# Kernel tuning notes

Hardware: AMD Instinct MI355X
Metric: run time of the kernel (lower is better)

Reference implementation:

```python
import jax, jax.numpy as jnp
import numpy as np

NUM_HEADS = 4
CATEGORY_SIZE = 128
DIM = 192
B, N, M = 2, 65000, 64


def setup_inputs() -> dict:
    key = jax.random.key(0)
    k1, k2, k3, k4 = jax.random.split(key, 4)
    qkv = jax.random.normal(k1, (B, N, 3 * DIM), dtype=jnp.float32)
    sim = jax.random.normal(k2, (B, N, M), dtype=jnp.float32)
    proj_w = jax.random.normal(k3, (DIM, DIM), dtype=jnp.float32) * (1.0 / np.sqrt(DIM))
    proj_b = jax.random.normal(k4, (DIM,), dtype=jnp.float32) * 0.01
    logit_scale = jnp.log(10.0 * jnp.ones((1, 1), dtype=jnp.float32))
    return {"qkv": qkv, "sim": sim, "proj_w": proj_w, "proj_b": proj_b,
            "logit_scale": logit_scale, "x_size": 65000}


def reference(qkv, sim, proj_w, proj_b, logit_scale, x_size):
    b, n, c3 = qkv.shape
    c = c3 // 3
    h = NUM_HEADS
    gs = min(n, CATEGORY_SIZE)
    ng = (n + gs - 1) // gs
    pad_n = ng * gs - n

    # token -> category id, then sort tokens by category
    tk_id = jnp.argmax(sim, axis=-1)                      # (b, n) int
    sort_idx = jnp.argsort(tk_id, axis=-1)                # (b, n)
    inv_idx = jnp.argsort(sort_idx, axis=-1)              # inverse permutation

    shuffled = jnp.take_along_axis(qkv, sort_idx[..., None], axis=1)  # (b, n, 3c)
    if pad_n > 0:
        pad = jnp.flip(shuffled[:, n - pad_n:n, :], axis=1)
        shuffled = jnp.concatenate([shuffled, pad], axis=1)           # (b, n+pad_n, 3c)

    # (3, b, ng, h, gs, c/h)
    y = shuffled.reshape(b, ng, gs, 3, h, c // h).transpose(3, 0, 1, 4, 2, 5)
    q, k, v = y[0], y[1], y[2]

    scale = jnp.exp(jnp.minimum(logit_scale, jnp.log(jnp.asarray(100.0, dtype=qkv.dtype))))
    attn = jnp.einsum('bghqd,bghkd->bghqk', q, k) * scale  # (b, ng, h, gs, gs)
    attn = jax.nn.softmax(attn, axis=-1)
    out = jnp.einsum('bghqk,bghkd->bghqd', attn, v)        # (b, ng, h, gs, c/h)
    out = out.transpose(0, 1, 3, 2, 4).reshape(b, n + pad_n, c)[:, :n, :]

    # scatter back to original token order
    out = jnp.take_along_axis(out, inv_idx[..., None], axis=1)
    return out @ proj_w.T + proj_b
```

## Files before the change

### kernel.cpp

```cpp
#include <hip/hip_runtime.h>
#include <hip/hip_bf16.h>
#include <math.h>

#define BB 2
#define NN 65000
#define MM 64
#define DIM 192
#define NH 4
#define HD 48
#define GS 128
#define NG 508
#define SORT_TPB 256
#define NBLK 254

#define NROWS_PAD 130048
#define NROWTILES 2032

typedef __attribute__((ext_vector_type(8))) short bf16x8;
typedef __attribute__((ext_vector_type(8))) _Float16 f16x8;
typedef __attribute__((ext_vector_type(2))) __fp16 fp16x2;
typedef __attribute__((ext_vector_type(4))) float f32x4;
typedef __attribute__((ext_vector_type(16))) float f32x16;
typedef __attribute__((ext_vector_type(8))) unsigned short u16x8;

__device__ __forceinline__ unsigned short f2bf(float f) {
  __hip_bfloat16 h = __float2bfloat16(f);
  return *(unsigned short*)&h;
}
__device__ __forceinline__ unsigned int pkh(float lo, float hi) {
  fp16x2 t = __builtin_amdgcn_cvt_pkrtz(lo, hi);
  return *(unsigned int*)&t;
}
__device__ __forceinline__ f16x8 cvt8h(float4 a, float4 b) {
  f16x8 r;
  r[0] = (_Float16)a.x; r[1] = (_Float16)a.y; r[2] = (_Float16)a.z; r[3] = (_Float16)a.w;
  r[4] = (_Float16)b.x; r[5] = (_Float16)b.y; r[6] = (_Float16)b.z; r[7] = (_Float16)b.w;
  return r;
}
__device__ __forceinline__ void gload_lds16(const float* src, float* lds_dst) {
  __builtin_amdgcn_global_load_lds(
      (const __attribute__((address_space(1))) unsigned int*)src,
      (__attribute__((address_space(3))) unsigned int*)lds_dst, 16, 0, 0);
}

__global__ void k_argmax_hist(const float* __restrict__ sim, int* __restrict__ tk,
                              int* __restrict__ hist) {
  __shared__ int cnt[MM];
  const int b = blockIdx.y, blk = blockIdx.x;
  if (threadIdx.x < MM) cnt[threadIdx.x] = 0;
  __syncthreads();
  int t = blk * SORT_TPB + threadIdx.x;
  if (t < NN) {
    const float4* row = (const float4*)(sim + ((size_t)b * NN + t) * MM);
    float best = -INFINITY;
    int bi = 0;
#pragma unroll
    for (int j = 0; j < MM / 4; ++j) {
      float4 v = row[j];
      if (v.x > best) { best = v.x; bi = 4 * j + 0; }
      if (v.y > best) { best = v.y; bi = 4 * j + 1; }
      if (v.z > best) { best = v.z; bi = 4 * j + 2; }
      if (v.w > best) { best = v.w; bi = 4 * j + 3; }
    }
    tk[b * NN + t] = bi;
    atomicAdd(&cnt[bi], 1);
  }
  __syncthreads();
  if (threadIdx.x < MM)
    hist[(b * NBLK + blk) * MM + threadIdx.x] = cnt[threadIdx.x];
}

__global__ void k_scan(const int* __restrict__ hist, int* __restrict__ boff) {
  const int b = blockIdx.x;
  const int tid = threadIdx.x;
  const int seg = tid >> 6, bin = tid & 63;
  __shared__ int part[4][MM];
  __shared__ int basev[MM];
  const int lo = seg * 64, hi = (seg == 3) ? NBLK : (lo + 64);
  int s = 0;
  for (int blk = lo; blk < hi; ++blk) s += hist[(b * NBLK + blk) * MM + bin];
  part[seg][bin] = s;
  __syncthreads();
  if (tid < 64) {
    int tot = part[0][bin] + part[1][bin] + part[2][bin] + part[3][bin];
    int incl = tot;
#pragma unroll
    for (int d = 1; d < 64; d <<= 1) {
      int o = __shfl_up(incl, d);
      if (bin >= d) incl += o;
    }
    basev[bin] = incl - tot;
  }
  __syncthreads();
  int run = basev[bin];
  for (int s2 = 0; s2 < seg; ++s2) run += part[s2][bin];
  for (int blk = lo; blk < hi; ++blk) {
    int h = hist[(b * NBLK + blk) * MM + bin];
    boff[(b * NBLK + blk) * MM + bin] = run;
    run += h;
  }
}

__global__ void k_scatter(const int* __restrict__ tk, const int* __restrict__ boff,
                          int* __restrict__ sidx) {
  __shared__ int whist[4][MM];
  const int b = blockIdx.y, blk = blockIdx.x;
  const int tid = threadIdx.x;
  const int w = tid >> 6, lane = tid & 63;
  ((int*)whist)[tid] = 0;
  __syncthreads();
  int t = blk * SORT_TPB + tid;
  int bin = (t < NN) ? tk[b * NN + t] : -1;
  unsigned long long m = ~0ull;
#pragma unroll
  for (int bit = 0; bit < 6; ++bit) {
    unsigned long long bl = __ballot((bin >> bit) & 1);
    m &= ((bin >> bit) & 1) ? bl : ~bl;
  }
  int rank_w = __popcll(m & ((1ull << lane) - 1ull));
  if (bin >= 0 && rank_w == 0) whist[w][bin] = __popcll(m);
  __syncthreads();
  if (bin >= 0) {
    int rank = rank_w;
#pragma unroll
    for (int w2 = 0; w2 < 3; ++w2)
      if (w2 < w) rank += whist[w2][bin];
    int pos = boff[(b * NBLK + blk) * MM + bin] + rank;
    sidx[b * NN + pos] = t;
  }
}

__global__ __launch_bounds__(256) void k_attn_mfma(const float* __restrict__ qkv,
                                                   const int* __restrict__ sidx,
                                                   const float* __restrict__ logit_scale,
                                                   __hip_bfloat16* __restrict__ attn_out) {
  const int x = blockIdx.x;
  const int g = ((x >> 5) << 3) + (x & 7);
  const int hd = (x >> 3) & 3;
  const int b = blockIdx.z;
  if (g >= NG) return;

  __shared__ int stok[GS];
  __shared__ _Float16 akv[4 * 3 * 64 * 8];
  __shared__ float vrowf[GS][HD];
  __shared__ _Float16 vfrag[2 * 8 * 64 * 8];

  const int tid = threadIdx.x;
  const int w = tid >> 6, l = tid & 63;
  const int hl = l >> 5, l31 = l & 31;

  if (tid < GS) {
    int s = g * GS + tid;
    int sp = (s < NN) ? s : (2 * NN - 1 - s);
    stok[tid] = sidx[b * NN + sp];
  }
  __syncthreads();

#pragma unroll
  for (int i = 0; i < 6; ++i) {
    int c = (i * 4 + w) * 64 + l;
    int row = c / 12, piece = c % 12;
    const float* src = qkv + (size_t)(b * NN + stok[row]) * (3 * DIM) + 2 * DIM + hd * HD + piece * 4;
    gload_lds16(src, &vrowf[0][0] + (i * 4 + w) * 256);
  }

  f16x8 qf[3];
  {
    const float* qsrc = qkv + (size_t)(b * NN + stok[w * 32 + l31]) * (3 * DIM) + hd * HD;
#pragma unroll
    for (int s = 0; s < 3; ++s) {
      const float4* p = (const float4*)(qsrc + s * 16 + hl * 8);
      qf[s] = cvt8h(p[0], p[1]);
    }
  }

#pragma unroll
  for (int i = 0; i < 3; ++i) {
    int c = tid + 256 * i;
    int ts = c >> 6, cl = c & 63;
    int kvr = (ts / 3) * 32 + (cl & 31);
    int dbase = (ts % 3) * 16 + (cl >> 5) * 8;
    const float* src = qkv + (size_t)(b * NN + stok[kvr]) * (3 * DIM) + DIM + hd * HD + dbase;
    ((f16x8*)akv)[c] = cvt8h(((const float4*)src)[0], ((const float4*)src)[1]);
  }
  __syncthreads();

#pragma unroll
  for (int i = 0; i < 4; ++i) {
    int c = tid + 256 * i;
    int ntks = c >> 6, cl = c & 63;
    int nt = ntks >> 3, ks = ntks & 7;
    int d = nt * 32 + (cl & 31);
    int kvb = ks * 16 + (cl >> 5) * 8;
    _Float16 tmp[8];
#pragma unroll
    for (int e = 0; e < 8; ++e) tmp[e] = (d < HD) ? (_Float16)vrowf[kvb + e][d] : (_Float16)0.f;
    ((f16x8*)vfrag)[c] = *(f16x8*)tmp;
  }
  __syncthreads();

  f32x16 accS[4];
#pragma unroll
  for (int t = 0; t < 4; ++t)
#pragma unroll
    for (int r = 0; r < 16; ++r) accS[t][r] = 0.f;

#pragma unroll
  for (int t = 0; t < 4; ++t)
#pragma unroll
    for (int s = 0; s < 3; ++s) {
      f16x8 af = ((const f16x8*)akv)[(t * 3 + s) * 64 + l];
      accS[t] = __builtin_amdgcn_mfma_f32_32x32x16_f16(af, qf[s], accS[t], 0, 0, 0);
    }

  const float scale = expf(fminf(logit_scale[0], 4.6051701860f));
  float mx = -INFINITY;
#pragma unroll
  for (int t = 0; t < 4; ++t)
#pragma unroll
    for (int r = 0; r < 16; ++r) { accS[t][r] *= scale; mx = fmaxf(mx, accS[t][r]); }
  mx = fmaxf(mx, __shfl_xor(mx, 32));
  float sum = 0.f;
#pragma unroll
  for (int t = 0; t < 4; ++t)
#pragma unroll
    for (int r = 0; r < 16; ++r) { float p = __expf(accS[t][r] - mx); accS[t][r] = p; sum += p; }
  sum += __shfl_xor(sum, 32);
  const float inv = 1.f / sum;
#pragma unroll
  for (int t = 0; t < 4; ++t)
#pragma unroll
    for (int r = 0; r < 16; ++r) accS[t][r] *= inv;

  f32x16 accO[2];
#pragma unroll
  for (int nt = 0; nt < 2; ++nt)
#pragma unroll
    for (int r = 0; r < 16; ++r) accO[nt][r] = 0.f;

#pragma unroll
  for (int t = 0; t < 4; ++t) {
    union { unsigned int u[4]; f16x8 v; } fa, fb;
    {
      unsigned int a0 = pkh(accS[t][0], accS[t][1]);
      unsigned int a1 = pkh(accS[t][2], accS[t][3]);
      unsigned int b0 = pkh(accS[t][4], accS[t][5]);
      unsigned int b1 = pkh(accS[t][6], accS[t][7]);
      unsigned int sa0 = __shfl_xor(a0, 32), sa1 = __shfl_xor(a1, 32);
      unsigned int sb0 = __shfl_xor(b0, 32), sb1 = __shfl_xor(b1, 32);
      fa.u[0] = hl ? sb0 : a0; fa.u[1] = hl ? sb1 : a1;
      fa.u[2] = hl ? b0 : sa0; fa.u[3] = hl ? b1 : sa1;
    }
    {
      unsigned int a0 = pkh(accS[t][8], accS[t][9]);
      unsigned int a1 = pkh(accS[t][10], accS[t][11]);
      unsigned int b0 = pkh(accS[t][12], accS[t][13]);
      unsigned int b1 = pkh(accS[t][14], accS[t][15]);
      unsigned int sa0 = __shfl_xor(a0, 32), sa1 = __shfl_xor(a1, 32);
      unsigned int sb0 = __shfl_xor(b0, 32), sb1 = __shfl_xor(b1, 32);
      fb.u[0] = hl ? sb0 : a0; fb.u[1] = hl ? sb1 : a1;
      fb.u[2] = hl ? b0 : sa0; fb.u[3] = hl ? b1 : sa1;
    }
    accO[0] = __builtin_amdgcn_mfma_f32_32x32x16_f16(fa.v, ((const f16x8*)vfrag)[(0 * 8 + 2 * t) * 64 + l], accO[0], 0, 0, 0);
    accO[1] = __builtin_amdgcn_mfma_f32_32x32x16_f16(fa.v, ((const f16x8*)vfrag)[(1 * 8 + 2 * t) * 64 + l], accO[1], 0, 0, 0);
    accO[0] = __builtin_amdgcn_mfma_f32_32x32x16_f16(fb.v, ((const f16x8*)vfrag)[(0 * 8 + 2 * t + 1) * 64 + l], accO[0], 0, 0, 0);
    accO[1] = __builtin_amdgcn_mfma_f32_32x32x16_f16(fb.v, ((const f16x8*)vfrag)[(1 * 8 + 2 * t + 1) * 64 + l], accO[1], 0, 0, 0);
  }

#pragma unroll
  for (int r = 0; r < 16; ++r) {
    int rowl = w * 32 + (r & 3) + 8 * (r >> 2) + 4 * hl;
    int sg = g * GS + rowl;
    if (sg < NN) {
      size_t base = (size_t)(b * NN + stok[rowl]) * DIM + hd * HD;
      attn_out[base + l31] = __float2bfloat16(accO[0][r]);
      if (l31 < 16) attn_out[base + 32 + l31] = __float2bfloat16(accO[1][r]);
    }
  }
}

__global__ void k_wpack(const float* __restrict__ W, unsigned short* __restrict__ wpack) {
  int idx = blockIdx.x * blockDim.x + threadIdx.x;
  if (idx >= 12 * 6 * 64) return;
  int lane = idx & 63;
  int kkjt = idx >> 6;
  int kk = kkjt % 6;
  int jt = kkjt / 6;
  int j = jt * 16 + (lane & 15);
  int k0 = kk * 32 + (lane >> 4) * 8;
  const float* src = W + (size_t)j * DIM + k0;
  unsigned short tmp[8];
#pragma unroll
  for (int e = 0; e < 8; ++e) tmp[e] = f2bf(src[e]);
  ((u16x8*)wpack)[idx] = *(const u16x8*)tmp;
}

__global__ __launch_bounds__(256) void k_proj_mfma(const unsigned short* __restrict__ xb,
                                                   const unsigned short* __restrict__ wpack,
                                                   const float* __restrict__ bias,
                                                   float* __restrict__ out) {
  __shared__ unsigned short wl[12 * 6 * 64 * 8];
  const int tid = threadIdx.x;

#pragma unroll
  for (int j = 0; j < 18; ++j) {
    int c = j * 256 + tid;
    gload_lds16((const float*)((const u16x8*)wpack + c), (float*)((u16x8*)wl + c));
  }

  const int wid = tid >> 6, lane = tid & 63;
  const int l15 = lane & 15, lk = lane >> 4;

  float bv[12];
#pragma unroll
  for (int jt = 0; jt < 12; ++jt) bv[jt] = bias[jt * 16 + l15];

  __syncthreads();

  for (int tile = blockIdx.x; tile < NROWTILES; tile += gridDim.x) {
    const int r0 = tile * 64 + wid * 16;
    f32x4 acc[12];
#pragma unroll
    for (int jt = 0; jt < 12; ++jt) { f32x4 t = {bv[jt], bv[jt], bv[jt], bv[jt]}; acc[jt] = t; }

    const unsigned short* xrow = xb + (size_t)(r0 + l15) * DIM;
#pragma unroll
    for (int kk = 0; kk < 6; ++kk) {
      bf16x8 a = *(const bf16x8*)(xrow + kk * 32 + lk * 8);
#pragma unroll
      for (int jt = 0; jt < 12; ++jt) {
        bf16x8 b = *(const bf16x8*)(wl + ((jt * 6 + kk) * 64 + lane) * 8);
        acc[jt] = __builtin_amdgcn_mfma_f32_16x16x32_bf16(a, b, acc[jt], 0, 0, 0);
      }
    }

    const int rowb = r0 + lk * 4;
#pragma unroll
    for (int jt = 0; jt < 12; ++jt) {
#pragma unroll
      for (int r = 0; r < 4; ++r) {
        int row = rowb + r;
        if (row < BB * NN)
          out[(size_t)row * DIM + jt * 16 + l15] = acc[jt][r];
      }
    }
  }
}

extern "C" void kernel_launch(void* const* d_in, const int* in_sizes, int n_in,
                              void* d_out, int out_size, void* d_ws, size_t ws_size,
                              hipStream_t stream) {
  const float* qkv = (const float*)d_in[0];
  const float* sim = (const float*)d_in[1];
  const float* proj_w = (const float*)d_in[2];
  const float* proj_b = (const float*)d_in[3];
  const float* logit_scale = (const float*)d_in[4];

  unsigned short* x_bf16 = (unsigned short*)d_ws;
  unsigned short* wpack = x_bf16 + (size_t)NROWS_PAD * DIM;
  int* tk = (int*)(wpack + 12 * 6 * 64 * 8);
  int* hist = tk + (size_t)BB * NN;
  int* boff = hist + (size_t)BB * NBLK * MM;
  int* sidx = boff + (size_t)BB * NBLK * MM;

  k_argmax_hist<<<dim3(NBLK, BB), SORT_TPB, 0, stream>>>(sim, tk, hist);
  k_scan<<<BB, 256, 0, stream>>>(hist, boff);
  k_scatter<<<dim3(NBLK, BB), SORT_TPB, 0, stream>>>(tk, boff, sidx);
  k_wpack<<<(12 * 6 * 64 + 255) / 256, 256, 0, stream>>>(proj_w, wpack);
  k_attn_mfma<<<dim3(2048, 1, BB), 256, 0, stream>>>(qkv, sidx, logit_scale,
                                                     (__hip_bfloat16*)x_bf16);
  k_proj_mfma<<<dim3(1016), 256, 0, stream>>>(x_bf16, wpack, proj_b, (float*)d_out);
}
```

Before: 160.1 us.

## Fuse attention and output projection into one kernel per group

Merges the per-head attention kernel and the projection GEMM into a single kernel. Each block handles one 128-token group and loops over all 4 heads, keeping the bf16 attention output in an LDS tile. It then runs the projection and scatters fp32 results to the original token positions. This removes the global bf16 intermediate round trip and one launch. The cost is only 1016 blocks with a serial head loop, V loaded with scalar gathers instead of async LDS loads, and projection weights read from global/L2 instead of LDS.

```diff
diff --git a/kernel.cpp b/kernel.cpp
--- a/kernel.cpp
+++ b/kernel.cpp
@@ -13,9 +13,6 @@
 #define SORT_TPB 256
 #define NBLK 254
 
-#define NROWS_PAD 130048
-#define NROWTILES 2032
-
 typedef __attribute__((ext_vector_type(8))) short bf16x8;
 typedef __attribute__((ext_vector_type(8))) _Float16 f16x8;
 typedef __attribute__((ext_vector_type(2))) __fp16 fp16x2;
@@ -36,11 +33,6 @@
   r[0] = (_Float16)a.x; r[1] = (_Float16)a.y; r[2] = (_Float16)a.z; r[3] = (_Float16)a.w;
   r[4] = (_Float16)b.x; r[5] = (_Float16)b.y; r[6] = (_Float16)b.z; r[7] = (_Float16)b.w;
   return r;
-}
-__device__ __forceinline__ void gload_lds16(const float* src, float* lds_dst) {
-  __builtin_amdgcn_global_load_lds(
-      (const __attribute__((address_space(1))) unsigned int*)src,
-      (__attribute__((address_space(3))) unsigned int*)lds_dst, 16, 0, 0);
 }
 
 __global__ void k_argmax_hist(const float* __restrict__ sim, int* __restrict__ tk,
@@ -127,155 +119,6 @@
       if (w2 < w) rank += whist[w2][bin];
     int pos = boff[(b * NBLK + blk) * MM + bin] + rank;
     sidx[b * NN + pos] = t;
-  }
-}
-
-__global__ __launch_bounds__(256) void k_attn_mfma(const float* __restrict__ qkv,
-                                                   const int* __restrict__ sidx,
-                                                   const float* __restrict__ logit_scale,
-                                                   __hip_bfloat16* __restrict__ attn_out) {
-  const int x = blockIdx.x;
-  const int g = ((x >> 5) << 3) + (x & 7);
-  const int hd = (x >> 3) & 3;
-  const int b = blockIdx.z;
-  if (g >= NG) return;
-
-  __shared__ int stok[GS];
-  __shared__ _Float16 akv[4 * 3 * 64 * 8];
-  __shared__ float vrowf[GS][HD];
-  __shared__ _Float16 vfrag[2 * 8 * 64 * 8];
-
-  const int tid = threadIdx.x;
-  const int w = tid >> 6, l = tid & 63;
-  const int hl = l >> 5, l31 = l & 31;
-
-  if (tid < GS) {
-    int s = g * GS + tid;
-    int sp = (s < NN) ? s : (2 * NN - 1 - s);
-    stok[tid] = sidx[b * NN + sp];
-  }
-  __syncthreads();
-
-#pragma unroll
-  for (int i = 0; i < 6; ++i) {
-    int c = (i * 4 + w) * 64 + l;
-    int row = c / 12, piece = c % 12;
-    const float* src = qkv + (size_t)(b * NN + stok[row]) * (3 * DIM) + 2 * DIM + hd * HD + piece * 4;
-    gload_lds16(src, &vrowf[0][0] + (i * 4 + w) * 256);
-  }
-
-  f16x8 qf[3];
-  {
-    const float* qsrc = qkv + (size_t)(b * NN + stok[w * 32 + l31]) * (3 * DIM) + hd * HD;
-#pragma unroll
-    for (int s = 0; s < 3; ++s) {
-      const float4* p = (const float4*)(qsrc + s * 16 + hl * 8);
-      qf[s] = cvt8h(p[0], p[1]);
-    }
-  }
-
-#pragma unroll
-  for (int i = 0; i < 3; ++i) {
-    int c = tid + 256 * i;
-    int ts = c >> 6, cl = c & 63;
-    int kvr = (ts / 3) * 32 + (cl & 31);
-    int dbase = (ts % 3) * 16 + (cl >> 5) * 8;
-    const float* src = qkv + (size_t)(b * NN + stok[kvr]) * (3 * DIM) + DIM + hd * HD + dbase;
-    ((f16x8*)akv)[c] = cvt8h(((const float4*)src)[0], ((const float4*)src)[1]);
-  }
-  __syncthreads();
-
-#pragma unroll
-  for (int i = 0; i < 4; ++i) {
-    int c = tid + 256 * i;
-    int ntks = c >> 6, cl = c & 63;
-    int nt = ntks >> 3, ks = ntks & 7;
-    int d = nt * 32 + (cl & 31);
-    int kvb = ks * 16 + (cl >> 5) * 8;
-    _Float16 tmp[8];
-#pragma unroll
-    for (int e = 0; e < 8; ++e) tmp[e] = (d < HD) ? (_Float16)vrowf[kvb + e][d] : (_Float16)0.f;
-    ((f16x8*)vfrag)[c] = *(f16x8*)tmp;
-  }
-  __syncthreads();
-
-  f32x16 accS[4];
-#pragma unroll
-  for (int t = 0; t < 4; ++t)
-#pragma unroll
-    for (int r = 0; r < 16; ++r) accS[t][r] = 0.f;
-
-#pragma unroll
-  for (int t = 0; t < 4; ++t)
-#pragma unroll
-    for (int s = 0; s < 3; ++s) {
-      f16x8 af = ((const f16x8*)akv)[(t * 3 + s) * 64 + l];
-      accS[t] = __builtin_amdgcn_mfma_f32_32x32x16_f16(af, qf[s], accS[t], 0, 0, 0);
-    }
-
-  const float scale = expf(fminf(logit_scale[0], 4.6051701860f));
-  float mx = -INFINITY;
-#pragma unroll
-  for (int t = 0; t < 4; ++t)
-#pragma unroll
-    for (int r = 0; r < 16; ++r) { accS[t][r] *= scale; mx = fmaxf(mx, accS[t][r]); }
-  mx = fmaxf(mx, __shfl_xor(mx, 32));
-  float sum = 0.f;
-#pragma unroll
-  for (int t = 0; t < 4; ++t)
-#pragma unroll
-    for (int r = 0; r < 16; ++r) { float p = __expf(accS[t][r] - mx); accS[t][r] = p; sum += p; }
-  sum += __shfl_xor(sum, 32);
-  const float inv = 1.f / sum;
-#pragma unroll
-  for (int t = 0; t < 4; ++t)
-#pragma unroll
-    for (int r = 0; r < 16; ++r) accS[t][r] *= inv;
-
-  f32x16 accO[2];
-#pragma unroll
-  for (int nt = 0; nt < 2; ++nt)
-#pragma unroll
-    for (int r = 0; r < 16; ++r) accO[nt][r] = 0.f;
-
-#pragma unroll
-  for (int t = 0; t < 4; ++t) {
-    union { unsigned int u[4]; f16x8 v; } fa, fb;
-    {
-      unsigned int a0 = pkh(accS[t][0], accS[t][1]);
-      unsigned int a1 = pkh(accS[t][2], accS[t][3]);
-      unsigned int b0 = pkh(accS[t][4], accS[t][5]);
-      unsigned int b1 = pkh(accS[t][6], accS[t][7]);
-      unsigned int sa0 = __shfl_xor(a0, 32), sa1 = __shfl_xor(a1, 32);
-      unsigned int sb0 = __shfl_xor(b0, 32), sb1 = __shfl_xor(b1, 32);
-      fa.u[0] = hl ? sb0 : a0; fa.u[1] = hl ? sb1 : a1;
-      fa.u[2] = hl ? b0 : sa0; fa.u[3] = hl ? b1 : sa1;
-    }
-    {
-      unsigned int a0 = pkh(accS[t][8], accS[t][9]);
-      unsigned int a1 = pkh(accS[t][10], accS[t][11]);
-      unsigned int b0 = pkh(accS[t][12], accS[t][13]);
-      unsigned int b1 = pkh(accS[t][14], accS[t][15]);
-      unsigned int sa0 = __shfl_xor(a0, 32), sa1 = __shfl_xor(a1, 32);
-      unsigned int sb0 = __shfl_xor(b0, 32), sb1 = __shfl_xor(b1, 32);
-      fb.u[0] = hl ? sb0 : a0; fb.u[1] = hl ? sb1 : a1;
-      fb.u[2] = hl ? b0 : sa0; fb.u[3] = hl ? b1 : sa1;
-    }
-    accO[0] = __builtin_amdgcn_mfma_f32_32x32x16_f16(fa.v, ((const f16x8*)vfrag)[(0 * 8 + 2 * t) * 64 + l], accO[0], 0, 0, 0);
-    accO[1] = __builtin_amdgcn_mfma_f32_32x32x16_f16(fa.v, ((const f16x8*)vfrag)[(1 * 8 + 2 * t) * 64 + l], accO[1], 0, 0, 0);
-    accO[0] = __builtin_amdgcn_mfma_f32_32x32x16_f16(fb.v, ((const f16x8*)vfrag)[(0 * 8 + 2 * t + 1) * 64 + l], accO[0], 0, 0, 0);
-    accO[1] = __builtin_amdgcn_mfma_f32_32x32x16_f16(fb.v, ((const f16x8*)vfrag)[(1 * 8 + 2 * t + 1) * 64 + l], accO[1], 0, 0, 0);
-  }
-
-#pragma unroll
-  for (int r = 0; r < 16; ++r) {
-    int rowl = w * 32 + (r & 3) + 8 * (r >> 2) + 4 * hl;
-    int sg = g * GS + rowl;
-    if (sg < NN) {
-      size_t base = (size_t)(b * NN + stok[rowl]) * DIM + hd * HD;
-      attn_out[base + l31] = __float2bfloat16(accO[0][r]);
-      if (l31 < 16) attn_out[base + 32 + l31] = __float2bfloat16(accO[1][r]);
-    }
   }
 }
 
@@ -295,42 +138,171 @@
   ((u16x8*)wpack)[idx] = *(const u16x8*)tmp;
 }
 
-__global__ __launch_bounds__(256) void k_proj_mfma(const unsigned short* __restrict__ xb,
+__global__ __launch_bounds__(256) void k_attn_proj(const float* __restrict__ qkv,
+                                                   const int* __restrict__ sidx,
+                                                   const float* __restrict__ logit_scale,
                                                    const unsigned short* __restrict__ wpack,
                                                    const float* __restrict__ bias,
                                                    float* __restrict__ out) {
-  __shared__ unsigned short wl[12 * 6 * 64 * 8];
+  const int g = blockIdx.x;
+  const int b = blockIdx.y;
+
+  __shared__ int stok[GS];
+  __shared__ __align__(16) _Float16 akv[4 * 3 * 64 * 8];
+  __shared__ __align__(16) _Float16 vfrag[2 * 8 * 64 * 8];
+  __shared__ __align__(16) unsigned short xtile[GS][200];
+
   const int tid = threadIdx.x;
-
-#pragma unroll
-  for (int j = 0; j < 18; ++j) {
-    int c = j * 256 + tid;
-    gload_lds16((const float*)((const u16x8*)wpack + c), (float*)((u16x8*)wl + c));
-  }
-
-  const int wid = tid >> 6, lane = tid & 63;
-  const int l15 = lane & 15, lk = lane >> 4;
-
+  const int w = tid >> 6, l = tid & 63;
+  const int hl = l >> 5, l31 = l & 31;
+
+  if (tid < GS) {
+    int s = g * GS + tid;
+    int sp = (s < NN) ? s : (2 * NN - 1 - s);
+    stok[tid] = sidx[b * NN + sp];
+  }
+  __syncthreads();
+
+  const float scale = expf(fminf(logit_scale[0], 4.6051701860f));
+
+  for (int hd = 0; hd < NH; ++hd) {
+    if (hd) __syncthreads();
+
+#pragma unroll
+    for (int i = 0; i < 3; ++i) {
+      int c = tid + 256 * i;
+      int ts = c >> 6, cl = c & 63;
+      int kvr = (ts / 3) * 32 + (cl & 31);
+      int dbase = (ts % 3) * 16 + (cl >> 5) * 8;
+      const float* src = qkv + (size_t)(b * NN + stok[kvr]) * (3 * DIM) + DIM + hd * HD + dbase;
+      ((f16x8*)akv)[c] = cvt8h(((const float4*)src)[0], ((const float4*)src)[1]);
+    }
+
+#pragma unroll
+    for (int i = 0; i < 4; ++i) {
+      int c = tid + 256 * i;
+      int ntks = c >> 6, cl = c & 63;
+      int nt = ntks >> 3, ks = ntks & 7;
+      int d = nt * 32 + (cl & 31);
+      int kvb = ks * 16 + (cl >> 5) * 8;
+      _Float16 tmp[8];
+      if (d < HD) {
+#pragma unroll
+        for (int e = 0; e < 8; ++e)
+          tmp[e] = (_Float16)qkv[(size_t)(b * NN + stok[kvb + e]) * (3 * DIM) + 2 * DIM + hd * HD + d];
+      } else {
+#pragma unroll
+        for (int e = 0; e < 8; ++e) tmp[e] = (_Float16)0.f;
+      }
+      ((f16x8*)vfrag)[c] = *(f16x8*)tmp;
+    }
+
+    f16x8 qf[3];
+    {
+      const float* qsrc = qkv + (size_t)(b * NN + stok[w * 32 + l31]) * (3 * DIM) + hd * HD;
+#pragma unroll
+      for (int s = 0; s < 3; ++s) {
+        const float4* p = (const float4*)(qsrc + s * 16 + hl * 8);
+        qf[s] = cvt8h(p[0], p[1]);
+      }
+    }
+    __syncthreads();
+
+    f32x16 accS[4];
+#pragma unroll
+    for (int t = 0; t < 4; ++t)
+#pragma unroll
+      for (int r = 0; r < 16; ++r) accS[t][r] = 0.f;
+
+#pragma unroll
+    for (int t = 0; t < 4; ++t)
+#pragma unroll
+      for (int s = 0; s < 3; ++s) {
+        f16x8 af = ((const f16x8*)akv)[(t * 3 + s) * 64 + l];
+        accS[t] = __builtin_amdgcn_mfma_f32_32x32x16_f16(af, qf[s], accS[t], 0, 0, 0);
+      }
+
+    float mx = -INFINITY;
+#pragma unroll
+    for (int t = 0; t < 4; ++t)
+#pragma unroll
+      for (int r = 0; r < 16; ++r) { accS[t][r] *= scale; mx = fmaxf(mx, accS[t][r]); }
+    mx = fmaxf(mx, __shfl_xor(mx, 32));
+    float sum = 0.f;
+#pragma unroll
+    for (int t = 0; t < 4; ++t)
+#pragma unroll
+      for (int r = 0; r < 16; ++r) { float p = __expf(accS[t][r] - mx); accS[t][r] = p; sum += p; }
+    sum += __shfl_xor(sum, 32);
+    const float inv = 1.f / sum;
+#pragma unroll
+    for (int t = 0; t < 4; ++t)
+#pragma unroll
+      for (int r = 0; r < 16; ++r) accS[t][r] *= inv;
+
+    f32x16 accO[2];
+#pragma unroll
+    for (int nt = 0; nt < 2; ++nt)
+#pragma unroll
+      for (int r = 0; r < 16; ++r) accO[nt][r] = 0.f;
+
+#pragma unroll
+    for (int t = 0; t < 4; ++t) {
+      union { unsigned int u[4]; f16x8 v; } fa, fb;
+      {
+        unsigned int a0 = pkh(accS[t][0], accS[t][1]);
+        unsigned int a1 = pkh(accS[t][2], accS[t][3]);
+        unsigned int b0 = pkh(accS[t][4], accS[t][5]);
+        unsigned int b1 = pkh(accS[t][6], accS[t][7]);
+        unsigned int sa0 = __shfl_xor(a0, 32), sa1 = __shfl_xor(a1, 32);
+        unsigned int sb0 = __shfl_xor(b0, 32), sb1 = __shfl_xor(b1, 32);
+        fa.u[0] = hl ? sb0 : a0; fa.u[1] = hl ? sb1 : a1;
+        fa.u[2] = hl ? b0 : sa0; fa.u[3] = hl ? b1 : sa1;
+      }
+      {
+        unsigned int a0 = pkh(accS[t][8], accS[t][9]);
+        unsigned int a1 = pkh(accS[t][10], accS[t][11]);
+        unsigned int b0 = pkh(accS[t][12], accS[t][13]);
+        unsigned int b1 = pkh(accS[t][14], accS[t][15]);
+        unsigned int sa0 = __shfl_xor(a0, 32), sa1 = __shfl_xor(a1, 32);
+        unsigned int sb0 = __shfl_xor(b0, 32), sb1 = __shfl_xor(b1, 32);
+        fb.u[0] = hl ? sb0 : a0; fb.u[1] = hl ? sb1 : a1;
+        fb.u[2] = hl ? b0 : sa0; fb.u[3] = hl ? b1 : sa1;
+      }
+      accO[0] = __builtin_amdgcn_mfma_f32_32x32x16_f16(fa.v, ((const f16x8*)vfrag)[(0 * 8 + 2 * t) * 64 + l], accO[0], 0, 0, 0);
+      accO[1] = __builtin_amdgcn_mfma_f32_32x32x16_f16(fa.v, ((const f16x8*)vfrag)[(1 * 8 + 2 * t) * 64 + l], accO[1], 0, 0, 0);
+      accO[0] = __builtin_amdgcn_mfma_f32_32x32x16_f16(fb.v, ((const f16x8*)vfrag)[(0 * 8 + 2 * t + 1) * 64 + l], accO[0], 0, 0, 0);
+      accO[1] = __builtin_amdgcn_mfma_f32_32x32x16_f16(fb.v, ((const f16x8*)vfrag)[(1 * 8 + 2 * t + 1) * 64 + l], accO[1], 0, 0, 0);
+    }
+
+#pragma unroll
+    for (int r = 0; r < 16; ++r) {
+      int rowl = w * 32 + (r & 3) + 8 * (r >> 2) + 4 * hl;
+      xtile[rowl][hd * HD + l31] = f2bf(accO[0][r]);
+      if (l31 < 16) xtile[rowl][hd * HD + 32 + l31] = f2bf(accO[1][r]);
+    }
+  }
+  __syncthreads();
+
+  const int l15 = l & 15, lk = l >> 4;
   float bv[12];
 #pragma unroll
   for (int jt = 0; jt < 12; ++jt) bv[jt] = bias[jt * 16 + l15];
 
-  __syncthreads();
-
-  for (int tile = blockIdx.x; tile < NROWTILES; tile += gridDim.x) {
-    const int r0 = tile * 64 + wid * 16;
+#pragma unroll
+  for (int grp = 0; grp < 2; ++grp) {
+    const int r0 = w * 32 + grp * 16;
     f32x4 acc[12];
 #pragma unroll
     for (int jt = 0; jt < 12; ++jt) { f32x4 t = {bv[jt], bv[jt], bv[jt], bv[jt]}; acc[jt] = t; }
 
-    const unsigned short* xrow = xb + (size_t)(r0 + l15) * DIM;
 #pragma unroll
     for (int kk = 0; kk < 6; ++kk) {
-      bf16x8 a = *(const bf16x8*)(xrow + kk * 32 + lk * 8);
+      bf16x8 a = *(const bf16x8*)&xtile[r0 + l15][kk * 32 + lk * 8];
 #pragma unroll
       for (int jt = 0; jt < 12; ++jt) {
-        bf16x8 b = *(const bf16x8*)(wl + ((jt * 6 + kk) * 64 + lane) * 8);
-        acc[jt] = __builtin_amdgcn_mfma_f32_16x16x32_bf16(a, b, acc[jt], 0, 0, 0);
+        bf16x8 bfr = *(const bf16x8*)(wpack + ((size_t)(jt * 6 + kk) * 64 + l) * 8);
+        acc[jt] = __builtin_amdgcn_mfma_f32_16x16x32_bf16(a, bfr, acc[jt], 0, 0, 0);
       }
     }
 
@@ -338,10 +310,11 @@
 #pragma unroll
     for (int jt = 0; jt < 12; ++jt) {
 #pragma unroll
-      for (int r = 0; r < 4; ++r) {
-        int row = rowb + r;
-        if (row < BB * NN)
-          out[(size_t)row * DIM + jt * 16 + l15] = acc[jt][r];
+      for (int rr = 0; rr < 4; ++rr) {
+        int row = rowb + rr;
+        int srow = g * GS + row;
+        if (srow < NN)
+          out[(size_t)(b * NN + stok[row]) * DIM + jt * 16 + l15] = acc[jt][rr];
       }
     }
   }
@@ -356,8 +329,7 @@
   const float* proj_b = (const float*)d_in[3];
   const float* logit_scale = (const float*)d_in[4];
 
-  unsigned short* x_bf16 = (unsigned short*)d_ws;
-  unsigned short* wpack = x_bf16 + (size_t)NROWS_PAD * DIM;
+  unsigned short* wpack = (unsigned short*)d_ws;
   int* tk = (int*)(wpack + 12 * 6 * 64 * 8);
   int* hist = tk + (size_t)BB * NN;
   int* boff = hist + (size_t)BB * NBLK * MM;
@@ -367,7 +339,6 @@
   k_scan<<<BB, 256, 0, stream>>>(hist, boff);
   k_scatter<<<dim3(NBLK, BB), SORT_TPB, 0, stream>>>(tk, boff, sidx);
   k_wpack<<<(12 * 6 * 64 + 255) / 256, 256, 0, stream>>>(proj_w, wpack);
-  k_attn_mfma<<<dim3(2048, 1, BB), 256, 0, stream>>>(qkv, sidx, logit_scale,
-                                                     (__hip_bfloat16*)x_bf16);
-  k_proj_mfma<<<dim3(1016), 256, 0, stream>>>(x_bf16, wpack, proj_b, (float*)d_out);
-}
+  k_attn_proj<<<dim3(NG, BB), 256, 0, stream>>>(qkv, sidx, logit_scale, wpack,
+                                                proj_b, (float*)d_out);
+}
```

Measured after the change: 214.5 us. +33.9%, slower.
